# Kernel optimization log

Measured on AMD Instinct MI355X. Metric: run time of the kernel, lower is better.

The kernel has to match this reference:

```python
import jax, jax.numpy as jnp
import numpy as np
import math

Z_DIM = 512
RADIUS = 64
K_TERMS = 700  # power-series length; ample for v=255, kappa<=800


def log_ive(v, x):
    """log(ive(v, x)) = log(I_v(x) * exp(-x)) via log-space power series.

    I_v(x) = sum_k (x/2)^(v+2k) / (k! * Gamma(v+k+1)); summed stably with
    logsumexp. x: [B,1] -> returns [B,1].
    """
    ks = jnp.arange(K_TERMS, dtype=x.dtype)
    # k-dependent log-gamma factors, shape [K]
    lg = jax.lax.lgamma(ks + 1.0) + jax.lax.lgamma(ks + v + 1.0)
    log_half_x = jnp.log(0.5 * x)                      # [B,1]
    terms = 2.0 * ks * log_half_x[..., None] - lg      # [B,1,K]
    return v * log_half_x + jax.nn.logsumexp(terms, axis=-1) - x


def setup_inputs() -> dict:
    key = jax.random.key(0)
    k1, k2, k3 = jax.random.split(key, 3)
    B, d = 65536, Z_DIM
    mu = jax.random.normal(k1, (B, d), dtype=jnp.float32)
    mu = mu / jnp.linalg.norm(mu, axis=1, keepdims=True)
    wc = jax.random.normal(k2, (B, d), dtype=jnp.float32)
    wc = wc / jnp.linalg.norm(wc, axis=1, keepdims=True) * RADIUS
    # realistic vMF concentrations
    kappa = jax.random.uniform(k3, (B, 1), dtype=jnp.float32) * 600.0 + 200.0
    return {"mu": mu, "kappa": kappa, "wc": wc}


def reference(mu, kappa, wc):
    d = float(Z_DIM)
    r = float(RADIUS)
    v = d / 2.0 - 1.0
    log_ive_kappa = jnp.log(1e-6 + jnp.exp(log_ive(v, kappa)))  # [B,1]
    log_iv_kappa = log_ive_kappa + kappa
    cos_theta = jnp.sum(mu * wc, axis=1, keepdims=True) / r      # [B,1]
    l1 = -kappa * cos_theta
    l2 = -(d / 2.0 - 1.0) * jnp.log(1e-6 + kappa)
    l3 = log_iv_kappa * 1.0
    losses = l1 + l2 + l3 + d / 2.0 * math.log(2.0 * math.pi) + d * math.log(r)
    return (losses, l1, l2, l3)
```

## Files before the change

### kernel.cpp

```cpp
#include <hip/hip_runtime.h>
#include <math.h>


#define K_TERMS 700
#define ZD 512
#define VV 255.0f
#define CONST_TERM 2599.8446676805443f

__global__ void lg_table_kernel(float* __restrict__ lg) {
    int i = blockIdx.x * blockDim.x + threadIdx.x;
    if (i < K_TERMS) {
        double k = (double)i;
        lg[i] = (float)(lgamma(k + 1.0) + lgamma(k + 256.0));
    }
}

__global__ __launch_bounds__(256) void vmf_kernel(
    const float* __restrict__ mu, const float* __restrict__ kappa,
    const float* __restrict__ wc, const float* __restrict__ lg,
    float* __restrict__ out, int B)
{
    const int wave = (int)((blockIdx.x * blockDim.x + threadIdx.x) >> 6);
    const int lane = (int)(threadIdx.x & 63);
    if (wave >= B) return;

    const float4* m4 = (const float4*)(mu + (size_t)wave * ZD) + lane * 2;
    const float4* w4 = (const float4*)(wc + (size_t)wave * ZD) + lane * 2;
    float4 a0 = m4[0], a1 = m4[1];
    float4 b0 = w4[0], b1 = w4[1];
    float dp = a0.x * b0.x + a0.y * b0.y + a0.z * b0.z + a0.w * b0.w
             + a1.x * b1.x + a1.y * b1.y + a1.z * b1.z + a1.w * b1.w;
    #pragma unroll
    for (int off = 32; off >= 1; off >>= 1)
        dp += __shfl_xor(dp, off, 64);

    const float kap = kappa[wave];
    const float L  = logf(0.5f * kap);

    float m = -3.4e38f, s = 0.0f;
    for (int k = lane; k < K_TERMS; k += 64) {
        float t = 2.0f * (float)k * L - lg[k];
        float nm = fmaxf(m, t);
        s = s * __expf(m - nm) + __expf(t - nm);
        m = nm;
    }
    #pragma unroll
    for (int off = 32; off >= 1; off >>= 1) {
        float mo = __shfl_xor(m, off, 64);
        float so = __shfl_xor(s, off, 64);
        float nm = fmaxf(m, mo);
        s = s * __expf(m - nm) + so * __expf(mo - nm);
        m = nm;
    }
    const float lse = m + logf(s);

    const float log_ive      = VV * L + lse - kap;
    const float log_ive_kap  = logf(1e-6f + __expf(log_ive));
    const float log_iv_kappa = log_ive_kap + kap;
    const float cos_theta    = dp * (1.0f / 64.0f);

    const float l1 = -kap * cos_theta;
    const float l2 = -VV * logf(1e-6f + kap);
    const float l3 = log_iv_kappa;
    const float losses = l1 + l2 + l3 + CONST_TERM;

    if (lane == 0) {
        out[wave]             = losses;
        out[(size_t)B + wave] = l1;
        out[(size_t)2 * B + wave] = l2;
        out[(size_t)3 * B + wave] = l3;
    }
}

extern "C" void kernel_launch(void* const* d_in, const int* in_sizes, int n_in,
                              void* d_out, int out_size, void* d_ws, size_t ws_size,
                              hipStream_t stream) {
    const float* mu    = (const float*)d_in[0];
    const float* kappa = (const float*)d_in[1];
    const float* wc    = (const float*)d_in[2];
    float* out = (float*)d_out;
    float* lg  = (float*)d_ws;
    const int B = in_sizes[1];

    lg_table_kernel<<<(K_TERMS + 255) / 256, 256, 0, stream>>>(lg);
    vmf_kernel<<<(B + 3) / 4, 256, 0, stream>>>(mu, kappa, wc, lg, out, B);
}
```

Before: 278.9 us.

## Sum only a 256-term window around the series peak; prefix-sum lgamma table

```diff
diff --git a/kernel.cpp b/kernel.cpp
--- a/kernel.cpp
+++ b/kernel.cpp
@@ -3,15 +3,41 @@
 
 
 #define K_TERMS 700
+#define WND 256
 #define ZD 512
 #define VV 255.0f
 #define CONST_TERM 2599.8446676805443f
 
-__global__ void lg_table_kernel(float* __restrict__ lg) {
-    int i = blockIdx.x * blockDim.x + threadIdx.x;
-    if (i < K_TERMS) {
-        double k = (double)i;
-        lg[i] = (float)(lgamma(k + 1.0) + lgamma(k + 256.0));
+__global__ __launch_bounds__(256) void lg_table_kernel(float* __restrict__ lg) {
+    __shared__ double ssum[256];
+    const int t = threadIdx.x;
+    double loc[3];
+    double tot = 0.0;
+    #pragma unroll
+    for (int i = 0; i < 3; ++i) {
+        int p = t * 3 + i;
+        double inc = 0.0;
+        if (p >= 1 && p < K_TERMS)
+            inc = log((double)p) + log((double)(p + 255));
+        tot += inc;
+        loc[i] = tot;
+    }
+    ssum[t] = tot;
+    __syncthreads();
+    for (int off = 1; off < 256; off <<= 1) {
+        double v = (t >= off) ? ssum[t - off] : 0.0;
+        __syncthreads();
+        ssum[t] += v;
+        __syncthreads();
+    }
+    const double excl = (t == 0) ? 0.0 : ssum[t - 1];
+    const double z = 256.0;
+    const double base = (z - 0.5) * log(z) - z + 0.918938533204672741780
+                      + 1.0 / (12.0 * z) - 1.0 / (360.0 * z * z * z);
+    #pragma unroll
+    for (int i = 0; i < 3; ++i) {
+        int p = t * 3 + i;
+        if (p < K_TERMS) lg[p] = (float)(base + excl + loc[i]);
     }
 }
 
@@ -28,31 +54,37 @@
     const float4* w4 = (const float4*)(wc + (size_t)wave * ZD) + lane * 2;
     float4 a0 = m4[0], a1 = m4[1];
     float4 b0 = w4[0], b1 = w4[1];
+
+    const float kap = kappa[wave];
+    const float L   = logf(0.5f * kap);
+
+    const float kstar = 0.5f * (sqrtf(65025.0f + kap * kap) - 255.0f);
+    int klo = (int)kstar - (WND / 2);
+    klo = klo < 0 ? 0 : (klo > (K_TERMS - WND) ? (K_TERMS - WND) : klo);
+
+    float t0, t1, t2, t3;
+    {
+        const int k0 = klo + lane;
+        t0 = fmaf(2.0f * (float)(k0),        L, -lg[k0]);
+        t1 = fmaf(2.0f * (float)(k0 + 64),   L, -lg[k0 + 64]);
+        t2 = fmaf(2.0f * (float)(k0 + 128),  L, -lg[k0 + 128]);
+        t3 = fmaf(2.0f * (float)(k0 + 192),  L, -lg[k0 + 192]);
+    }
+    float m = fmaxf(fmaxf(t0, t1), fmaxf(t2, t3));
+    #pragma unroll
+    for (int off = 32; off >= 1; off >>= 1)
+        m = fmaxf(m, __shfl_xor(m, off, 64));
+    float s = __expf(t0 - m) + __expf(t1 - m) + __expf(t2 - m) + __expf(t3 - m);
+    #pragma unroll
+    for (int off = 32; off >= 1; off >>= 1)
+        s += __shfl_xor(s, off, 64);
+    const float lse = m + logf(s);
+
     float dp = a0.x * b0.x + a0.y * b0.y + a0.z * b0.z + a0.w * b0.w
              + a1.x * b1.x + a1.y * b1.y + a1.z * b1.z + a1.w * b1.w;
     #pragma unroll
     for (int off = 32; off >= 1; off >>= 1)
         dp += __shfl_xor(dp, off, 64);
-
-    const float kap = kappa[wave];
-    const float L  = logf(0.5f * kap);
-
-    float m = -3.4e38f, s = 0.0f;
-    for (int k = lane; k < K_TERMS; k += 64) {
-        float t = 2.0f * (float)k * L - lg[k];
-        float nm = fmaxf(m, t);
-        s = s * __expf(m - nm) + __expf(t - nm);
-        m = nm;
-    }
-    #pragma unroll
-    for (int off = 32; off >= 1; off >>= 1) {
-        float mo = __shfl_xor(m, off, 64);
-        float so = __shfl_xor(s, off, 64);
-        float nm = fmaxf(m, mo);
-        s = s * __expf(m - nm) + so * __expf(mo - nm);
-        m = nm;
-    }
-    const float lse = m + logf(s);
 
     const float log_ive      = VV * L + lse - kap;
     const float log_ive_kap  = logf(1e-6f + __expf(log_ive));
@@ -65,8 +97,8 @@
     const float losses = l1 + l2 + l3 + CONST_TERM;
 
     if (lane == 0) {
-        out[wave]             = losses;
-        out[(size_t)B + wave] = l1;
+        out[wave]                 = losses;
+        out[(size_t)B + wave]     = l1;
         out[(size_t)2 * B + wave] = l2;
         out[(size_t)3 * B + wave] = l3;
     }
@@ -82,6 +114,6 @@
     float* lg  = (float*)d_ws;
     const int B = in_sizes[1];
 
-    lg_table_kernel<<<(K_TERMS + 255) / 256, 256, 0, stream>>>(lg);
+    lg_table_kernel<<<1, 256, 0, stream>>>(lg);
     vmf_kernel<<<(B + 3) / 4, 256, 0, stream>>>(mu, kappa, wc, lg, out, B);
 }
```

Result: no change. 276.9 us (-0.7%).
